# Kernel tuning notes

Measured on AMD Instinct MI355X. Metric: run time of the kernel, lower is better.

## Reference

```python
import jax, jax.numpy as jnp
import numpy as np

N, E, D = 100000, 1600000, 128
EPS = 1e-5


def setup_inputs() -> dict:
    key = jax.random.key(0)
    ks = jax.random.split(key, 8)
    inp = {
        "feats": jax.random.normal(ks[0], (N, D), dtype=jnp.float32),
        "src": jax.random.randint(ks[1], (E,), 0, N, dtype=jnp.int64) if jax.config.jax_enable_x64 else jax.random.randint(ks[1], (E,), 0, N, dtype=jnp.int32),
        "dst": jax.random.randint(ks[2], (E,), 0, N, dtype=jnp.int32),
        "W0": jax.random.normal(ks[3], (D, D), dtype=jnp.float32) / np.sqrt(D),
        "b0": jnp.zeros((D,), jnp.float32),
        "rW0": jax.random.normal(ks[4], (D, D), dtype=jnp.float32) / np.sqrt(D),
        "rb0": jnp.zeros((D,), jnp.float32),
        "g0": jnp.ones((D,), jnp.float32),
        "beta0": jnp.zeros((D,), jnp.float32),
        "W1": jax.random.normal(ks[5], (D, D), dtype=jnp.float32) / np.sqrt(D),
        "b1": jnp.zeros((D,), jnp.float32),
        "rW1": jax.random.normal(ks[6], (D, D), dtype=jnp.float32) / np.sqrt(D),
        "rb1": jnp.zeros((D,), jnp.float32),
        "g1": jnp.ones((D,), jnp.float32),
        "beta1": jnp.zeros((D,), jnp.float32),
    }
    return inp


def gcn_layer(x, src, dst, W, b, rW, rb, gamma, beta):
    # GraphConv(norm='none'): project then sum over in-edges, + bias, relu
    m = x @ W                                   # [N, D]
    agg = jax.ops.segment_sum(m[src], dst, num_segments=x.shape[0])  # [N, D]
    h = jax.nn.relu(agg + b)
    # residual: relu(Linear(x))
    h = h + jax.nn.relu(x @ rW + rb)
    # dropout p=0 -> identity; BatchNorm1d (training batch stats, biased var)
    mu = h.mean(axis=0)
    var = h.var(axis=0)
    return (h - mu) * jax.lax.rsqrt(var + EPS) * gamma + beta


def reference(feats, src, dst, W0, b0, rW0, rb0, g0, beta0,
              W1, b1, rW1, rb1, g1, beta1):
    h = gcn_layer(feats, src, dst, W0, b0, rW0, rb0, g0, beta0)
    h = gcn_layer(h, src, dst, W1, b1, rW1, rb1, g1, beta1)
    return h
```

## Files before the change

### kernel.cpp

```cpp
#include <hip/hip_runtime.h>
#include <hip/hip_bf16.h>
#include <cstdint>

#define N_NODES 100000
#define N_EDGES 1600000
#define DD 128

#define NC 196
#define CSHIFT 9
#define CMASK 511
#define EPB 8192
#define NPB 196
#define FCAP 9216

typedef float f32x4 __attribute__((ext_vector_type(4)));
typedef __bf16 bf16x8 __attribute__((ext_vector_type(8)));

union ABFrag { uint4 u4; uint16_t us[8]; bf16x8 v; };

__device__ __forceinline__ float bf2f(uint16_t u) {
  return __uint_as_float(((uint32_t)u) << 16);
}
__device__ __forceinline__ uint16_t f2bf(float f) {
  uint32_t u = __float_as_uint(f);
  uint32_t r = (u + 0x7fffu + ((u >> 16) & 1u)) >> 16;
  return (uint16_t)r;
}

__global__ __launch_bounds__(256) void hist_coarse_k(const int* __restrict__ dst,
                                                     int* __restrict__ ch) {
  __shared__ int lh[NC];
  if (threadIdx.x < NC) lh[threadIdx.x] = 0;
  __syncthreads();
  int stride = gridDim.x * blockDim.x;
  for (int e = blockIdx.x * blockDim.x + threadIdx.x; e < N_EDGES; e += stride)
    atomicAdd(&lh[dst[e] >> CSHIFT], 1);
  __syncthreads();
  if (threadIdx.x < NC) atomicAdd(&ch[threadIdx.x], lh[threadIdx.x]);
}

__global__ __launch_bounds__(256) void scan_coarse_k(const int* __restrict__ ch,
                                                     int* __restrict__ coff,
                                                     int* __restrict__ gcursor) {
  __shared__ int s[NC];
  if (threadIdx.x < NC) s[threadIdx.x] = ch[threadIdx.x];
  __syncthreads();
  if (threadIdx.x == 0) {
    int run = 0;
    for (int i = 0; i < NC; ++i) { coff[i] = run; gcursor[i] = run; run += s[i]; }
    coff[NC] = run;
  }
}

__global__ __launch_bounds__(256) void partition_k(const int* __restrict__ src,
                                                   const int* __restrict__ dst,
                                                   int* __restrict__ gcursor,
                                                   uint32_t* __restrict__ ec) {
  __shared__ int lhist[NC];
  __shared__ int lscan[NC + 1];
  __shared__ int lcur[NC];
  __shared__ int gbase[NC];
  __shared__ uint32_t staged[EPB];
  const int tid = threadIdx.x;
  const int b0 = blockIdx.x * EPB;
  const int cnt = min(EPB, N_EDGES - b0);
  if (tid < NC) lhist[tid] = 0;
  __syncthreads();
  for (int i = tid; i < cnt; i += 256)
    atomicAdd(&lhist[dst[b0 + i] >> CSHIFT], 1);
  __syncthreads();
  if (tid == 0) {
    int run = 0;
    for (int c = 0; c < NC; ++c) { lscan[c] = run; run += lhist[c]; }
    lscan[NC] = run;
  }
  __syncthreads();
  if (tid < NC) {
    lcur[tid] = lscan[tid];
    gbase[tid] = atomicAdd(&gcursor[tid], lhist[tid]);
  }
  __syncthreads();
  for (int i = tid; i < cnt; i += 256) {
    int d = dst[b0 + i];
    int c = d >> CSHIFT;
    int p = atomicAdd(&lcur[c], 1);
    staged[p] = ((uint32_t)src[b0 + i] << CSHIFT) | (uint32_t)(d & CMASK);
  }
  __syncthreads();
  for (int i = tid; i < cnt; i += 256) {
    int lo = 0, hi = NC - 1;
    while (lo < hi) {
      int mid = (lo + hi + 1) >> 1;
      if (lscan[mid] <= i) lo = mid; else hi = mid - 1;
    }
    ec[gbase[lo] + (i - lscan[lo])] = staged[i];
  }
}

__global__ __launch_bounds__(256) void finesort_k(const int* __restrict__ coff,
                                                  const uint32_t* __restrict__ ec,
                                                  uint32_t* __restrict__ ef,
                                                  int* __restrict__ row_ptr) {
  __shared__ int h[512];
  __shared__ int sc[513];
  __shared__ int cur[512];
  __shared__ int wsum[4];
  __shared__ uint32_t staged[FCAP];
  const int tid = threadIdx.x;
  const int c = blockIdx.x;
  const int base = coff[c];
  const int cnt = coff[c + 1] - base;
  h[tid] = 0; h[tid + 256] = 0;
  __syncthreads();
  for (int i = tid; i < cnt; i += 256)
    atomicAdd(&h[ec[base + i] & CMASK], 1);
  __syncthreads();
  {
    int a = h[2 * tid], b = h[2 * tid + 1];
    int s = a + b;
    int ln = tid & 63, w = tid >> 6;
    int incl = s;
    #pragma unroll
    for (int o = 1; o < 64; o <<= 1) {
      int t2 = __shfl_up(incl, o);
      if (ln >= o) incl += t2;
    }
    if (ln == 63) wsum[w] = incl;
    __syncthreads();
    int woff = 0;
    #pragma unroll
    for (int i = 0; i < 4; ++i) if (i < w) woff += wsum[i];
    int exc = woff + incl - s;
    sc[2 * tid] = exc;
    sc[2 * tid + 1] = exc + a;
    if (tid == 255) sc[512] = woff + incl;
  }
  __syncthreads();
  cur[tid] = sc[tid]; cur[tid + 256] = sc[tid + 256];
  __syncthreads();
  for (int i = tid; i < cnt; i += 256) {
    uint32_t u = ec[base + i];
    int p = atomicAdd(&cur[u & CMASK], 1);
    if (p < FCAP) staged[p] = u >> CSHIFT;
  }
  __syncthreads();
  for (int i = tid; i < cnt; i += 256) ef[base + i] = staged[i];
  for (int n = tid; n < 512; n += 256) {
    int v = c * 512 + n;
    if (v < N_NODES) row_ptr[v] = base + sc[n];
  }
  if (c == 0 && tid == 0) row_ptr[N_NODES] = N_EDGES;
}

__global__ __launch_bounds__(64) void wprep_k(const float* __restrict__ w0, const float* __restrict__ rw0,
                                              const float* __restrict__ w1, const float* __restrict__ rw1,
                                              uint16_t* __restrict__ wfrag) {
  int b = blockIdx.x;
  int o = b >> 5, s = (b >> 3) & 3, t = b & 7, l = threadIdx.x;
  const float* W = (o == 0) ? w0 : (o == 1) ? rw0 : (o == 2) ? w1 : rw1;
  #pragma unroll
  for (int i = 0; i < 8; ++i) {
    int k = s * 32 + ((l >> 4) << 3) + i;
    int cc = t * 16 + (l & 15);
    wfrag[((size_t)b * 64 + l) * 8 + i] = f2bf(W[k * DD + cc]);
  }
}

template <bool AFFINE>
__global__ __launch_bounds__(256) void gemm_dual(
    const float* __restrict__ xf,
    const uint32_t* __restrict__ xb,
    const float2* __restrict__ afin,
    const uint4* __restrict__ wfragL,
    const float* __restrict__ rbias,
    uint16_t* __restrict__ mo, uint16_t* __restrict__ ro) {
  const int w = threadIdx.x >> 6, l = threadIdx.x & 63;
  const int row0 = blockIdx.x * 64 + w * 16;
  const int rload = min(row0 + (l & 15), N_NODES - 1);
  const int kg = (l >> 4) * 8;
  ABFrag a[4];
  #pragma unroll
  for (int s = 0; s < 4; ++s) {
    const int k0 = s * 32 + kg;
    if (!AFFINE) {
      const float4* p = (const float4*)(xf + (size_t)rload * DD + k0);
      float4 x0 = p[0], x1 = p[1];
      a[s].us[0] = f2bf(x0.x); a[s].us[1] = f2bf(x0.y);
      a[s].us[2] = f2bf(x0.z); a[s].us[3] = f2bf(x0.w);
      a[s].us[4] = f2bf(x1.x); a[s].us[5] = f2bf(x1.y);
      a[s].us[6] = f2bf(x1.z); a[s].us[7] = f2bf(x1.w);
    } else {
      uint4 hv = *(const uint4*)(xb + (size_t)rload * 64 + k0 / 2);
      uint32_t hu[4] = {hv.x, hv.y, hv.z, hv.w};
      #pragma unroll
      for (int q = 0; q < 4; ++q) {
        int cc = k0 + 2 * q;
        float2 A0 = afin[cc], A1 = afin[cc + 1];
        float f0 = bf2f((uint16_t)hu[q]) * A0.x + A0.y;
        float f1 = bf2f((uint16_t)(hu[q] >> 16)) * A1.x + A1.y;
        a[s].us[2 * q] = f2bf(f0);
        a[s].us[2 * q + 1] = f2bf(f1);
      }
    }
  }
  const int colb = l & 15;
  const int rbase = row0 + (l >> 4) * 4;
  #pragma unroll
  for (int oo = 0; oo < 2; ++oo) {
    #pragma unroll
    for (int t = 0; t < 8; ++t) {
      f32x4 acc = {0.f, 0.f, 0.f, 0.f};
      #pragma unroll
      for (int s = 0; s < 4; ++s) {
        ABFrag bfr;
        bfr.u4 = wfragL[((oo * 4 + s) * 8 + t) * 64 + l];
        acc = __builtin_amdgcn_mfma_f32_16x16x32_bf16(a[s].v, bfr.v, acc, 0, 0, 0);
      }
      const int col = t * 16 + colb;
      if (oo == 0) {
        #pragma unroll
        for (int rr = 0; rr < 4; ++rr) {
          int rowo = rbase + rr;
          if (rowo < N_NODES) mo[(size_t)rowo * DD + col] = f2bf(acc[rr]);
        }
      } else {
        float rbv = rbias[col];
        #pragma unroll
        for (int rr = 0; rr < 4; ++rr) {
          int rowo = rbase + rr;
          if (rowo < N_NODES) ro[(size_t)rowo * DD + col] = f2bf(fmaxf(acc[rr] + rbv, 0.f));
        }
      }
    }
  }
}

__global__ __launch_bounds__(256) void agg_node_k(
    const int* __restrict__ row_ptr, const uint32_t* __restrict__ ef,
    const uint32_t* __restrict__ m2, const uint32_t* __restrict__ r2,
    const float* __restrict__ bias, uint32_t* __restrict__ h2,
    float* __restrict__ stats) {
  const int w = threadIdx.x >> 6, l = threadIdx.x & 63;
  const int gw = blockIdx.x * 4 + w;
  const int nw = gridDim.x * 4;
  const float bb0 = bias[2 * l], bb1 = bias[2 * l + 1];
  float ls0 = 0.f, lsq0 = 0.f, ls1 = 0.f, lsq1 = 0.f;
  for (int v = gw; v < N_NODES; v += nw) {
    const int j0 = row_ptr[v], j1 = row_ptr[v + 1];
    float a0 = 0.f, a1 = 0.f;
    int j = j0;
    for (; j + 8 <= j1; j += 8) {
      int s0 = ef[j], s1 = ef[j + 1], s2 = ef[j + 2], s3 = ef[j + 3];
      int s4 = ef[j + 4], s5 = ef[j + 5], s6 = ef[j + 6], s7 = ef[j + 7];
      uint32_t u0 = m2[(size_t)s0 * 64 + l];
      uint32_t u1 = m2[(size_t)s1 * 64 + l];
      uint32_t u2 = m2[(size_t)s2 * 64 + l];
      uint32_t u3 = m2[(size_t)s3 * 64 + l];
      uint32_t u4 = m2[(size_t)s4 * 64 + l];
      uint32_t u5 = m2[(size_t)s5 * 64 + l];
      uint32_t u6 = m2[(size_t)s6 * 64 + l];
      uint32_t u7 = m2[(size_t)s7 * 64 + l];
      a0 += bf2f((uint16_t)u0) + bf2f((uint16_t)u1) + bf2f((uint16_t)u2) + bf2f((uint16_t)u3)
          + bf2f((uint16_t)u4) + bf2f((uint16_t)u5) + bf2f((uint16_t)u6) + bf2f((uint16_t)u7);
      a1 += bf2f((uint16_t)(u0 >> 16)) + bf2f((uint16_t)(u1 >> 16)) + bf2f((uint16_t)(u2 >> 16))
          + bf2f((uint16_t)(u3 >> 16)) + bf2f((uint16_t)(u4 >> 16)) + bf2f((uint16_t)(u5 >> 16))
          + bf2f((uint16_t)(u6 >> 16)) + bf2f((uint16_t)(u7 >> 16));
    }
    for (; j < j1; ++j) {
      uint32_t u = m2[(size_t)((uint32_t)ef[j]) * 64 + l];
      a0 += bf2f((uint16_t)u);
      a1 += bf2f((uint16_t)(u >> 16));
    }
    uint32_t rv = r2[(size_t)v * 64 + l];
    float h0v = fmaxf(a0 + bb0, 0.f) + bf2f((uint16_t)rv);
    float h1v = fmaxf(a1 + bb1, 0.f) + bf2f((uint16_t)(rv >> 16));
    h2[(size_t)v * 64 + l] = (uint32_t)f2bf(h0v) | ((uint32_t)f2bf(h1v) << 16);
    ls0 += h0v; lsq0 += h0v * h0v;
    ls1 += h1v; lsq1 += h1v * h1v;
  }
  __shared__ float red[4][128];
  red[w][2 * l] = ls0; red[w][2 * l + 1] = ls1;
  __syncthreads();
  if (threadIdx.x < 128) {
    float s = red[0][threadIdx.x] + red[1][threadIdx.x] + red[2][threadIdx.x] + red[3][threadIdx.x];
    atomicAdd(&stats[threadIdx.x], s);
  }
  __syncthreads();
  red[w][2 * l] = lsq0; red[w][2 * l + 1] = lsq1;
  __syncthreads();
  if (threadIdx.x < 128) {
    float s = red[0][threadIdx.x] + red[1][threadIdx.x] + red[2][threadIdx.x] + red[3][threadIdx.x];
    atomicAdd(&stats[128 + threadIdx.x], s);
  }
}

__global__ void affine_k(const float* __restrict__ stats, const float* __restrict__ g,
                         const float* __restrict__ beta, float2* __restrict__ af) {
  int c = threadIdx.x;
  float mu = stats[c] / (float)N_NODES;
  float var = stats[128 + c] / (float)N_NODES - mu * mu;
  float sc = g[c] * rsqrtf(var + 1e-5f);
  af[c] = make_float2(sc, beta[c] - mu * sc);
}

__global__ __launch_bounds__(256) void bn_out(const uint2* __restrict__ h4,
                                              const float2* __restrict__ af1,
                                              float4* __restrict__ out4) {
  int stride = gridDim.x * blockDim.x;
  for (int i = blockIdx.x * blockDim.x + threadIdx.x; i < N_NODES * 32; i += stride) {
    uint2 u = h4[i];
    int c0 = (i & 31) * 4;
    float2 A0 = af1[c0], A1 = af1[c0 + 1], A2 = af1[c0 + 2], A3 = af1[c0 + 3];
    float4 o;
    o.x = bf2f((uint16_t)u.x) * A0.x + A0.y;
    o.y = bf2f((uint16_t)(u.x >> 16)) * A1.x + A1.y;
    o.z = bf2f((uint16_t)u.y) * A2.x + A2.y;
    o.w = bf2f((uint16_t)(u.y >> 16)) * A3.x + A3.y;
    out4[i] = o;
  }
}

extern "C" void kernel_launch(void* const* d_in, const int* in_sizes, int n_in,
                              void* d_out, int out_size, void* d_ws, size_t ws_size,
                              hipStream_t stream) {
  const float* feats = (const float*)d_in[0];
  const int* srcI = (const int*)d_in[1];
  const int* dstI = (const int*)d_in[2];
  const float* W0 = (const float*)d_in[3];
  const float* b0 = (const float*)d_in[4];
  const float* rW0 = (const float*)d_in[5];
  const float* rb0 = (const float*)d_in[6];
  const float* g0 = (const float*)d_in[7];
  const float* be0 = (const float*)d_in[8];
  const float* W1 = (const float*)d_in[9];
  const float* b1 = (const float*)d_in[10];
  const float* rW1 = (const float*)d_in[11];
  const float* rb1 = (const float*)d_in[12];
  const float* g1 = (const float*)d_in[13];
  const float* be1 = (const float*)d_in[14];
  float* out = (float*)d_out;

  char* ws = (char*)d_ws;
  size_t off = 0;
  auto alloc = [&](size_t bytes) {
    size_t r = off;
    off += (bytes + 255) & ~(size_t)255;
    return r;
  };
  uint16_t* wfrag = (uint16_t*)(ws + alloc(65536 * 2));
  float* stats = (float*)(ws + alloc(512 * 4));
  float2* af = (float2*)(ws + alloc(256 * 8));
  int* ch = (int*)(ws + alloc(NC * 4));
  int* coff = (int*)(ws + alloc((NC + 1) * 4));
  int* gcursor = (int*)(ws + alloc(NC * 4));
  int* row_ptr = (int*)(ws + alloc((N_NODES + 1) * 4));
  uint32_t* ec = (uint32_t*)(ws + alloc((size_t)N_EDGES * 4));
  uint32_t* ef = (uint32_t*)(ws + alloc((size_t)N_EDGES * 4));
  uint16_t* mb = (uint16_t*)(ws + alloc((size_t)N_NODES * DD * 2));
  uint16_t* rbuf = (uint16_t*)(ws + alloc((size_t)N_NODES * DD * 2));
  uint16_t* hb = (uint16_t*)(ws + alloc((size_t)N_NODES * DD * 2));

  hipMemsetAsync(ch, 0, NC * 4, stream);
  hipMemsetAsync(stats, 0, 512 * 4, stream);

  hist_coarse_k<<<392, 256, 0, stream>>>(dstI, ch);
  scan_coarse_k<<<1, 256, 0, stream>>>(ch, coff, gcursor);
  partition_k<<<NPB, 256, 0, stream>>>(srcI, dstI, gcursor, ec);
  finesort_k<<<NC, 256, 0, stream>>>(coff, ec, ef, row_ptr);
  wprep_k<<<128, 64, 0, stream>>>(W0, rW0, W1, rW1, wfrag);

  const int gemm_grid = (N_NODES + 63) / 64;
  gemm_dual<false><<<gemm_grid, 256, 0, stream>>>(feats, nullptr, nullptr, (const uint4*)wfrag,
                                                  rb0, mb, rbuf);
  agg_node_k<<<2048, 256, 0, stream>>>(row_ptr, ef, (const uint32_t*)mb, (const uint32_t*)rbuf,
                                       b0, (uint32_t*)hb, stats);
  affine_k<<<1, 128, 0, stream>>>(stats, g0, be0, af);
  gemm_dual<true><<<gemm_grid, 256, 0, stream>>>(nullptr, (const uint32_t*)hb, af,
                                                 (const uint4*)(wfrag + 32768), rb1, mb, rbuf);
  agg_node_k<<<2048, 256, 0, stream>>>(row_ptr, ef, (const uint32_t*)mb, (const uint32_t*)rbuf,
                                       b1, (uint32_t*)hb, stats + 256);
  affine_k<<<1, 128, 0, stream>>>(stats + 256, g1, be1, af + 128);
  bn_out<<<2048, 256, 0, stream>>>((const uint2*)hb, af + 128, (float4*)out);
}
```

Before: 509.5 us.

## Finer sort buckets, bucket-id tagging in partition, LDS-staged coalesced GEMM stores

Halves the coarse bucket width (256 nodes per bucket, 391 buckets) and halves the partition block size. This lets the fine-sort blocks work on smaller chunks and spreads the sort across more blocks. The partition kernel records each staged edge's bucket id in shared memory instead of binary-searching the scan for every element. The dual GEMM now keeps all 16 accumulators and writes the bf16 outputs through an LDS tile, so global stores become 16-byte row-contiguous writes instead of scattered 2-byte ones. This raises register pressure and LDS use in the GEMM, and it drops the row clamp because it assumes full 16-row tiles, which holds since N is divisible by 16.

```diff
diff --git a/kernel.cpp b/kernel.cpp
--- a/kernel.cpp
+++ b/kernel.cpp
@@ -6,12 +6,12 @@
 #define N_EDGES 1600000
 #define DD 128
 
-#define NC 196
-#define CSHIFT 9
-#define CMASK 511
-#define EPB 8192
-#define NPB 196
-#define FCAP 9216
+#define NC 391
+#define CSHIFT 8
+#define CMASK 255
+#define EPB 4096
+#define NPB 391
+#define FCAP 4608
 
 typedef float f32x4 __attribute__((ext_vector_type(4)));
 typedef __bf16 bf16x8 __attribute__((ext_vector_type(8)));
@@ -30,20 +30,20 @@
 __global__ __launch_bounds__(256) void hist_coarse_k(const int* __restrict__ dst,
                                                      int* __restrict__ ch) {
   __shared__ int lh[NC];
-  if (threadIdx.x < NC) lh[threadIdx.x] = 0;
+  for (int i = threadIdx.x; i < NC; i += 256) lh[i] = 0;
   __syncthreads();
   int stride = gridDim.x * blockDim.x;
   for (int e = blockIdx.x * blockDim.x + threadIdx.x; e < N_EDGES; e += stride)
     atomicAdd(&lh[dst[e] >> CSHIFT], 1);
   __syncthreads();
-  if (threadIdx.x < NC) atomicAdd(&ch[threadIdx.x], lh[threadIdx.x]);
+  for (int i = threadIdx.x; i < NC; i += 256) atomicAdd(&ch[i], lh[i]);
 }
 
 __global__ __launch_bounds__(256) void scan_coarse_k(const int* __restrict__ ch,
                                                      int* __restrict__ coff,
                                                      int* __restrict__ gcursor) {
   __shared__ int s[NC];
-  if (threadIdx.x < NC) s[threadIdx.x] = ch[threadIdx.x];
+  for (int i = threadIdx.x; i < NC; i += 256) s[i] = ch[i];
   __syncthreads();
   if (threadIdx.x == 0) {
     int run = 0;
@@ -57,14 +57,15 @@
                                                    int* __restrict__ gcursor,
                                                    uint32_t* __restrict__ ec) {
   __shared__ int lhist[NC];
-  __shared__ int lscan[NC + 1];
+  __shared__ int lscan[NC];
   __shared__ int lcur[NC];
   __shared__ int gbase[NC];
   __shared__ uint32_t staged[EPB];
+  __shared__ uint16_t cbuck[EPB];
   const int tid = threadIdx.x;
   const int b0 = blockIdx.x * EPB;
   const int cnt = min(EPB, N_EDGES - b0);
-  if (tid < NC) lhist[tid] = 0;
+  for (int i = tid; i < NC; i += 256) lhist[i] = 0;
   __syncthreads();
   for (int i = tid; i < cnt; i += 256)
     atomicAdd(&lhist[dst[b0 + i] >> CSHIFT], 1);
@@ -72,12 +73,11 @@
   if (tid == 0) {
     int run = 0;
     for (int c = 0; c < NC; ++c) { lscan[c] = run; run += lhist[c]; }
-    lscan[NC] = run;
-  }
-  __syncthreads();
-  if (tid < NC) {
-    lcur[tid] = lscan[tid];
-    gbase[tid] = atomicAdd(&gcursor[tid], lhist[tid]);
+  }
+  __syncthreads();
+  for (int i = tid; i < NC; i += 256) {
+    lcur[i] = lscan[i];
+    gbase[i] = atomicAdd(&gcursor[i], lhist[i]);
   }
   __syncthreads();
   for (int i = tid; i < cnt; i += 256) {
@@ -85,15 +85,12 @@
     int c = d >> CSHIFT;
     int p = atomicAdd(&lcur[c], 1);
     staged[p] = ((uint32_t)src[b0 + i] << CSHIFT) | (uint32_t)(d & CMASK);
+    cbuck[p] = (uint16_t)c;
   }
   __syncthreads();
   for (int i = tid; i < cnt; i += 256) {
-    int lo = 0, hi = NC - 1;
-    while (lo < hi) {
-      int mid = (lo + hi + 1) >> 1;
-      if (lscan[mid] <= i) lo = mid; else hi = mid - 1;
-    }
-    ec[gbase[lo] + (i - lscan[lo])] = staged[i];
+    int c = cbuck[i];
+    ec[gbase[c] + (i - lscan[c])] = staged[i];
   }
 }
 
@@ -101,25 +98,24 @@
                                                   const uint32_t* __restrict__ ec,
                                                   uint32_t* __restrict__ ef,
                                                   int* __restrict__ row_ptr) {
-  __shared__ int h[512];
-  __shared__ int sc[513];
-  __shared__ int cur[512];
+  __shared__ int h[256];
+  __shared__ int sc[257];
+  __shared__ int cur[256];
   __shared__ int wsum[4];
   __shared__ uint32_t staged[FCAP];
   const int tid = threadIdx.x;
   const int c = blockIdx.x;
   const int base = coff[c];
   const int cnt = coff[c + 1] - base;
-  h[tid] = 0; h[tid + 256] = 0;
+  h[tid] = 0;
   __syncthreads();
   for (int i = tid; i < cnt; i += 256)
     atomicAdd(&h[ec[base + i] & CMASK], 1);
   __syncthreads();
   {
-    int a = h[2 * tid], b = h[2 * tid + 1];
-    int s = a + b;
+    int a = h[tid];
     int ln = tid & 63, w = tid >> 6;
-    int incl = s;
+    int incl = a;
     #pragma unroll
     for (int o = 1; o < 64; o <<= 1) {
       int t2 = __shfl_up(incl, o);
@@ -130,13 +126,11 @@
     int woff = 0;
     #pragma unroll
     for (int i = 0; i < 4; ++i) if (i < w) woff += wsum[i];
-    int exc = woff + incl - s;
-    sc[2 * tid] = exc;
-    sc[2 * tid + 1] = exc + a;
-    if (tid == 255) sc[512] = woff + incl;
-  }
-  __syncthreads();
-  cur[tid] = sc[tid]; cur[tid + 256] = sc[tid + 256];
+    sc[tid] = woff + incl - a;
+    if (tid == 255) sc[256] = woff + incl;
+  }
+  __syncthreads();
+  cur[tid] = sc[tid];
   __syncthreads();
   for (int i = tid; i < cnt; i += 256) {
     uint32_t u = ec[base + i];
@@ -145,9 +139,9 @@
   }
   __syncthreads();
   for (int i = tid; i < cnt; i += 256) ef[base + i] = staged[i];
-  for (int n = tid; n < 512; n += 256) {
-    int v = c * 512 + n;
-    if (v < N_NODES) row_ptr[v] = base + sc[n];
+  {
+    int v = c * 256 + tid;
+    if (v < N_NODES) row_ptr[v] = base + sc[tid];
   }
   if (c == 0 && tid == 0) row_ptr[N_NODES] = N_EDGES;
 }
@@ -174,9 +168,11 @@
     const uint4* __restrict__ wfragL,
     const float* __restrict__ rbias,
     uint16_t* __restrict__ mo, uint16_t* __restrict__ ro) {
+  __shared__ uint16_t lt[4][16][136];
   const int w = threadIdx.x >> 6, l = threadIdx.x & 63;
   const int row0 = blockIdx.x * 64 + w * 16;
-  const int rload = min(row0 + (l & 15), N_NODES - 1);
+  if (row0 >= N_NODES) return;
+  const int rload = row0 + (l & 15);
   const int kg = (l >> 4) * 8;
   ABFrag a[4];
   #pragma unroll
@@ -204,33 +200,44 @@
     }
   }
   const int colb = l & 15;
-  const int rbase = row0 + (l >> 4) * 4;
+  const int rgrp = l >> 4;
+  float rbl[8];
+  #pragma unroll
+  for (int t = 0; t < 8; ++t) rbl[t] = rbias[t * 16 + colb];
+  f32x4 accs[16];
+  #pragma unroll
+  for (int i = 0; i < 16; ++i) accs[i] = f32x4{0.f, 0.f, 0.f, 0.f};
   #pragma unroll
   for (int oo = 0; oo < 2; ++oo) {
     #pragma unroll
     for (int t = 0; t < 8; ++t) {
-      f32x4 acc = {0.f, 0.f, 0.f, 0.f};
       #pragma unroll
       for (int s = 0; s < 4; ++s) {
         ABFrag bfr;
         bfr.u4 = wfragL[((oo * 4 + s) * 8 + t) * 64 + l];
-        acc = __builtin_amdgcn_mfma_f32_16x16x32_bf16(a[s].v, bfr.v, acc, 0, 0, 0);
+        accs[oo * 8 + t] =
+            __builtin_amdgcn_mfma_f32_16x16x32_bf16(a[s].v, bfr.v, accs[oo * 8 + t], 0, 0, 0);
       }
-      const int col = t * 16 + colb;
-      if (oo == 0) {
-        #pragma unroll
-        for (int rr = 0; rr < 4; ++rr) {
-          int rowo = rbase + rr;
-          if (rowo < N_NODES) mo[(size_t)rowo * DD + col] = f2bf(acc[rr]);
-        }
-      } else {
-        float rbv = rbias[col];
-        #pragma unroll
-        for (int rr = 0; rr < 4; ++rr) {
-          int rowo = rbase + rr;
-          if (rowo < N_NODES) ro[(size_t)rowo * DD + col] = f2bf(fmaxf(acc[rr] + rbv, 0.f));
-        }
+    }
+  }
+  #pragma unroll
+  for (int oo = 0; oo < 2; ++oo) {
+    #pragma unroll
+    for (int t = 0; t < 8; ++t) {
+      f32x4 acc = accs[oo * 8 + t];
+      #pragma unroll
+      for (int rr = 0; rr < 4; ++rr) {
+        float v = acc[rr];
+        if (oo == 1) v = fmaxf(v + rbl[t], 0.f);
+        lt[w][rgrp * 4 + rr][t * 16 + colb] = f2bf(v);
       }
+    }
+    uint16_t* dstm = (oo == 0) ? mo : ro;
+    #pragma unroll
+    for (int i = 0; i < 4; ++i) {
+      int row = i * 4 + rgrp;
+      uint4 val = *(const uint4*)((const char*)&lt[w][0][0] + row * 272 + colb * 16);
+      *(uint4*)((char*)dstm + (size_t)(row0 + row) * 256 + colb * 16) = val;
     }
   }
 }
@@ -363,7 +370,7 @@
   hipMemsetAsync(ch, 0, NC * 4, stream);
   hipMemsetAsync(stats, 0, 512 * 4, stream);
 
-  hist_coarse_k<<<392, 256, 0, stream>>>(dstI, ch);
+  hist_coarse_k<<<784, 256, 0, stream>>>(dstI, ch);
   scan_coarse_k<<<1, 256, 0, stream>>>(ch, coff, gcursor);
   partition_k<<<NPB, 256, 0, stream>>>(srcI, dstI, gcursor, ec);
   finesort_k<<<NC, 256, 0, stream>>>(coff, ec, ef, row_ptr);
```

After: 517.0 us. No clear change (+1.5%).
